# Performance work log

Hardware: AMD Instinct MI355X
Metric: run time of the kernel (lower is better)

## Reference

```python
import jax, jax.numpy as jnp
import numpy as np

B, NQ, NK = 2, 2048, 2048
QD, CD, H, DH = 1024, 768, 16, 64
INNER = H * DH


def setup_inputs() -> dict:
    key = jax.random.key(0)
    ks = jax.random.split(key, 8)
    x = jax.random.normal(ks[0], (B, NQ, QD), jnp.float32)
    context = jax.random.normal(ks[1], (B, NK, CD), jnp.float32)
    mask = jax.random.randint(ks[2], (B, 1, NQ, NK), 0, 2) > 0
    s = lambda d: 1.0 / np.sqrt(d)
    Wq = jax.random.normal(ks[3], (INNER, QD), jnp.float32) * s(QD)
    Wk = jax.random.normal(ks[4], (INNER, CD), jnp.float32) * s(CD)
    Wv = jax.random.normal(ks[5], (INNER, CD), jnp.float32) * s(CD)
    Wo = jax.random.normal(ks[6], (QD, INNER), jnp.float32) * s(INNER)
    bo = jax.random.normal(ks[7], (QD,), jnp.float32) * 0.01
    return {"x": x, "context": context, "mask": mask,
            "Wq": Wq, "Wk": Wk, "Wv": Wv, "Wo": Wo, "bo": bo}


def reference(x, context, mask, Wq, Wk, Wv, Wo, bo):
    scale = DH ** -0.5
    # QKV projections (Linear, no bias): [b, n, inner] -> [b, n, h, d]
    q = (x @ Wq.T).reshape(B, NQ, H, DH)
    k = (context @ Wk.T).reshape(B, NK, H, DH)
    v = (context @ Wv.T).reshape(B, NK, H, DH)
    # additive bias built from boolean mask (masked_fill with -finfo.max/2)
    max_neg = -jnp.finfo(q.dtype).max / 2
    bias = jnp.where(mask, jnp.zeros((), q.dtype), max_neg)  # [b,1,nq,nk]
    scores = jnp.einsum('bqhd,bkhd->bhqk', q, k) * scale + bias
    attn = jax.nn.softmax(scores, axis=-1)
    out = jnp.einsum('bhqk,bkhd->bqhd', attn, v).reshape(B, NQ, INNER)
    return out @ Wo.T + bo
```

## Files before the change

### kernel.cpp

```cpp
#include <hip/hip_runtime.h>
#include <float.h>
#include <stdint.h>

#define C_B     2
#define C_NQ    2048
#define C_NK    2048
#define C_QD    1024
#define C_CD    768
#define C_H     16
#define C_DH    64
#define C_INNER 1024

typedef __bf16 bf16;
typedef __attribute__((ext_vector_type(8))) __bf16 bf16x8;
typedef __attribute__((ext_vector_type(4))) __bf16 bf16x4;
typedef __attribute__((ext_vector_type(4))) float f32x4;
typedef __attribute__((ext_vector_type(16))) float f32x16;

#if __has_builtin(__builtin_amdgcn_exp2f)
#define EXP2(x) __builtin_amdgcn_exp2f(x)
#else
#define EXP2(x) __expf((x) * 0.69314718056f)
#endif

__device__ __forceinline__ void async_copy16(const bf16* g, bf16* l) {
  __builtin_amdgcn_global_load_lds(
      (const __attribute__((address_space(1))) void*)g,
      (__attribute__((address_space(3))) void*)l,
      16, 0, 0);
}

__global__ __launch_bounds__(256) void prep(const float* __restrict__ s0, const float* __restrict__ s1,
                                            const float* __restrict__ s2, const float* __restrict__ s3,
                                            const float* __restrict__ s4, const float* __restrict__ s5,
                                            bf16* __restrict__ d0, bf16* __restrict__ d1,
                                            bf16* __restrict__ d2, bf16* __restrict__ d3,
                                            bf16* __restrict__ d4, bf16* __restrict__ d5,
                                            const int* __restrict__ mask,
                                            unsigned long long* __restrict__ mb) {
  const int stride = gridDim.x * blockDim.x;
  for (int idx = blockIdx.x * blockDim.x + threadIdx.x; idx < 2752512; idx += stride) {
    const float* src; bf16* dst; int loc;
    if      (idx < 1048576) { src = s0; dst = d0; loc = idx; }
    else if (idx < 1835008) { src = s1; dst = d1; loc = idx - 1048576; }
    else if (idx < 2097152) { src = s2; dst = d2; loc = idx - 1835008; }
    else if (idx < 2293760) { src = s3; dst = d3; loc = idx - 2097152; }
    else if (idx < 2490368) { src = s4; dst = d4; loc = idx - 2293760; }
    else                    { src = s5; dst = d5; loc = idx - 2490368; }
    float4 f = *(const float4*)&src[loc * 4];
    bf16x4 o = { (bf16)f.x, (bf16)f.y, (bf16)f.z, (bf16)f.w };
    *(bf16x4*)&dst[loc * 4] = o;
  }
  const int lane = threadIdx.x & 63;
  const int wid  = (blockIdx.x * blockDim.x + threadIdx.x) >> 6;
  const int nw   = (gridDim.x * blockDim.x) >> 6;
  for (int w = wid; w < 131072; w += nw) {
    int v = mask[(size_t)w * 64 + lane];
    unsigned long long bb = __ballot(v != 0);
    if (lane == 0) mb[w] = bb;
  }
}

__device__ __forceinline__ void gemm_core(const bf16* __restrict__ A,
                                          const bf16* __restrict__ W,
                                          int m0, int n0, int K,
                                          bf16* As0, bf16* As1, bf16* Bs0, bf16* Bs1,
                                          f32x4 (&acc)[4][4],
                                          int w, int lane) {
  const int l15 = lane & 15, lg = lane >> 4;
  const int wm = w >> 1, wn = w & 1;
  bf16* AsA[2] = {As0, As1};
  bf16* BsA[2] = {Bs0, Bs1};

  auto stage = [&](int nb, int k0) {
#pragma unroll
    for (int i = 0; i < 2; ++i) {
      const int chunk = w * 128 + i * 64 + lane;
      const int row = chunk >> 2;
      const int srcb = ((chunk & 3) ^ (row & 3)) * 8;
      async_copy16(A + (size_t)(m0 + row) * K + k0 + srcb, &AsA[nb][chunk * 8]);
      async_copy16(W + (size_t)(n0 + row) * K + k0 + srcb, &BsA[nb][chunk * 8]);
    }
  };

  stage(0, 0);
  int cur = 0;
  for (int k0 = 0; k0 < K; k0 += 32) {
    __syncthreads();
    if (k0 + 32 < K) stage(cur ^ 1, k0 + 32);

    bf16x8 af[4], bfv[4];
#pragma unroll
    for (int mi = 0; mi < 4; ++mi) {
      const int row = wm * 64 + mi * 16 + l15;
      af[mi] = *(const bf16x8*)&AsA[cur][row * 32 + ((lg ^ (row & 3)) * 8)];
    }
#pragma unroll
    for (int ni = 0; ni < 4; ++ni) {
      const int row = wn * 64 + ni * 16 + l15;
      bfv[ni] = *(const bf16x8*)&BsA[cur][row * 32 + ((lg ^ (row & 3)) * 8)];
    }
#pragma unroll
    for (int mi = 0; mi < 4; ++mi)
#pragma unroll
      for (int ni = 0; ni < 4; ++ni)
        acc[mi][ni] = __builtin_amdgcn_mfma_f32_16x16x32_bf16(af[mi], bfv[ni],
                                                              acc[mi][ni], 0, 0, 0);
    cur ^= 1;
  }
}

__global__ __launch_bounds__(256) void gemm_qkv(const bf16* __restrict__ xb,
                                                const bf16* __restrict__ wqb,
                                                bf16* __restrict__ Qb,
                                                const bf16* __restrict__ cb,
                                                const bf16* __restrict__ wkv,
                                                bf16* __restrict__ Kb,
                                                bf16* __restrict__ Vb,
                                                float qscale) {
  __shared__ __align__(16) bf16 As[2][128 * 32];
  __shared__ __align__(16) bf16 Bs[2][128 * 32];

  const int bid = blockIdx.x;
  const int t = threadIdx.x, w = t >> 6, lane = t & 63;
  const int l15 = lane & 15, lg = lane >> 4;
  const int wm = w >> 1, wn = w & 1;

  const bf16 *A, *W;
  int m0, n0, K;
  float oscale;
  if (bid < 256) {
    A = xb; W = wqb; n0 = (bid & 7) * 128; m0 = (bid >> 3) * 128;
    K = C_QD; oscale = qscale;
  } else {
    const int b2 = bid - 256;
    A = cb; W = wkv; n0 = (b2 & 15) * 128; m0 = (b2 >> 4) * 128;
    K = C_CD; oscale = 1.0f;
  }

  f32x4 acc[4][4] = {};
  gemm_core(A, W, m0, n0, K, As[0], As[1], Bs[0], Bs[1], acc, w, lane);

#pragma unroll
  for (int mi = 0; mi < 4; ++mi)
#pragma unroll
    for (int ni = 0; ni < 4; ++ni)
#pragma unroll
      for (int r = 0; r < 4; ++r) {
        const int row = m0 + wm * 64 + mi * 16 + lg * 4 + r;
        const int col = n0 + wn * 64 + ni * 16 + l15;
        const float v = acc[mi][ni][r] * oscale;
        bf16* dst; int cc;
        if (bid < 256)            { dst = Qb; cc = col; }
        else if (col < C_INNER)   { dst = Kb; cc = col; }
        else                      { dst = Vb; cc = col - C_INNER; }
        dst[(size_t)row * C_INNER + cc] = (bf16)v;
      }
}

__global__ __launch_bounds__(256) void gemm_out(const bf16* __restrict__ A,
                                                const bf16* __restrict__ W,
                                                const float* __restrict__ bias,
                                                float* __restrict__ Cout,
                                                int M, int N, int K) {
  __shared__ __align__(16) bf16 As[2][64 * 32];
  __shared__ __align__(16) bf16 Bs[2][128 * 32];
  const int t = threadIdx.x, w = t >> 6, lane = t & 63;
  const int l15 = lane & 15, lg = lane >> 4;
  const int wm = w >> 1, wn = w & 1;
  const int m0 = blockIdx.y * 64, n0 = blockIdx.x * 128;

  f32x4 acc[2][4] = {};

  auto stage = [&](int nb, int k0) {
    {
      const int ca = w * 64 + lane;
      const int arow = ca >> 2;
      const int asrc = ((ca & 3) ^ (arow & 3)) * 8;
      async_copy16(A + (size_t)(m0 + arow) * K + k0 + asrc, &As[nb][ca * 8]);
    }
#pragma unroll
    for (int i = 0; i < 2; ++i) {
      const int cbk = w * 128 + i * 64 + lane;
      const int brow = cbk >> 2;
      const int bsrc = ((cbk & 3) ^ (brow & 3)) * 8;
      async_copy16(W + (size_t)(n0 + brow) * K + k0 + bsrc, &Bs[nb][cbk * 8]);
    }
  };

  stage(0, 0);
  int cur = 0;
  for (int k0 = 0; k0 < K; k0 += 32) {
    __syncthreads();
    if (k0 + 32 < K) stage(cur ^ 1, k0 + 32);

    bf16x8 af[2], bfv[4];
#pragma unroll
    for (int mi = 0; mi < 2; ++mi) {
      const int row = wm * 32 + mi * 16 + l15;
      af[mi] = *(const bf16x8*)&As[cur][row * 32 + ((lg ^ (row & 3)) * 8)];
    }
#pragma unroll
    for (int ni = 0; ni < 4; ++ni) {
      const int row = wn * 64 + ni * 16 + l15;
      bfv[ni] = *(const bf16x8*)&Bs[cur][row * 32 + ((lg ^ (row & 3)) * 8)];
    }
#pragma unroll
    for (int mi = 0; mi < 2; ++mi)
#pragma unroll
      for (int ni = 0; ni < 4; ++ni)
        acc[mi][ni] = __builtin_amdgcn_mfma_f32_16x16x32_bf16(af[mi], bfv[ni],
                                                              acc[mi][ni], 0, 0, 0);
    cur ^= 1;
  }

#pragma unroll
  for (int mi = 0; mi < 2; ++mi)
#pragma unroll
    for (int ni = 0; ni < 4; ++ni)
#pragma unroll
      for (int r = 0; r < 4; ++r) {
        const int row = m0 + wm * 32 + mi * 16 + lg * 4 + r;
        const int col = n0 + wn * 64 + ni * 16 + l15;
        Cout[(size_t)row * N + col] = acc[mi][ni][r] + bias[col];
      }
}

__global__ __launch_bounds__(256) void vtrans(const bf16* __restrict__ V,
                                              bf16* __restrict__ Vt) {
  __shared__ __align__(16) bf16 T[64][80];
  const int kt = blockIdx.x, h = blockIdx.y, b = blockIdx.z;
  const int t = threadIdx.x;
  {
    const int kl = t >> 2, db = (t & 3) * 16;
    const bf16* src = &V[((size_t)(b * C_NK + kt * 64 + kl)) * C_INNER + h * 64 + db];
    *(bf16x8*)&T[kl][db]     = *(const bf16x8*)&src[0];
    *(bf16x8*)&T[kl][db + 8] = *(const bf16x8*)&src[8];
  }
  __syncthreads();
  {
    const int d = t >> 2, kb = (t & 3) * 16;
    const int P0[8] = {0, 1, 2, 3, 8, 9, 10, 11};
    const int P1[8] = {4, 5, 6, 7, 12, 13, 14, 15};
    bf16x8 o0, o1;
#pragma unroll
    for (int j = 0; j < 8; ++j) { o0[j] = T[kb + P0[j]][d]; o1[j] = T[kb + P1[j]][d]; }
    bf16* dst = &Vt[((size_t)((b * C_H + h) * C_DH + d)) * C_NK + kt * 64 + kb];
    *(bf16x8*)&dst[0] = o0;
    *(bf16x8*)&dst[8] = o1;
  }
}

__global__ __launch_bounds__(256, 4) void attn_fwd(const bf16* __restrict__ Q,
                                                   const bf16* __restrict__ K,
                                                   const bf16* __restrict__ Vt,
                                                   const unsigned long long* __restrict__ MB,
                                                   bf16* __restrict__ O0,
                                                   bf16* __restrict__ O1,
                                                   float* __restrict__ L) {
  __shared__ __align__(16) bf16 Ks[2][64 * 64];
  __shared__ __align__(16) bf16 Vs[2][64 * 64];

  const int bid = blockIdx.x;
  const int swz = ((bid & 7) << 7) | (bid >> 3);
  const int qt = swz & 15, h = (swz >> 4) & 15, zz = swz >> 8;
  const int half = zz >> 1, b = zz & 1;
  const int t = threadIdx.x, wq = t >> 6, lane = t & 63;
  const int l31 = lane & 31, hi = lane >> 5;
  const int q = qt * 128 + wq * 32 + l31;

  bf16x8 qf[4];
  {
    const bf16* qp = Q + ((size_t)(b * C_NQ + q)) * C_INNER + h * C_DH;
#pragma unroll
    for (int db = 0; db < 4; ++db)
      qf[db] = *(const bf16x8*)&qp[db * 16 + hi * 8];
  }

  float l_run = 0.f;
  f32x16 acc_o[2] = {};

  auto stage = [&](int nb, int ktA) {
#pragma unroll
    for (int i = 0; i < 2; ++i) {
      const int chunk = wq * 128 + i * 64 + lane;
      const int row = chunk >> 3, pcb = chunk & 7;
      const int srcb = (pcb ^ (row & 7)) * 8;
      const bf16* kg = K + ((size_t)(b * C_NK + ktA * 64 + row)) * C_INNER + h * C_DH + srcb;
      async_copy16(kg, &Ks[nb][chunk * 8]);
      const bf16* vg = Vt + ((size_t)((b * C_H + h) * C_DH + row)) * C_NK + ktA * 64 + srcb;
      async_copy16(vg, &Vs[nb][chunk * 8]);
    }
  };

  const int kt0 = half * 16;
  stage(0, kt0);
  int cur = 0;

  for (int i = 0; i < 16; ++i) {
    const int ktA = kt0 + i;
    const unsigned long long wd =
        MB[((size_t)(b * C_NQ + q)) * (C_NK / 64) + ktA] >> (hi * 4);
    const unsigned mlo = (unsigned)wd, mhi = (unsigned)(wd >> 32);

    __syncthreads();
    if (i + 1 < 16) stage(cur ^ 1, ktA + 1);

    f32x16 s[2] = {};
    __builtin_amdgcn_s_setprio(1);
#pragma unroll
    for (int kb = 0; kb < 2; ++kb)
#pragma unroll
      for (int db = 0; db < 4; ++db) {
        const int row = kb * 32 + l31;
        const int cb = (db * 2 + hi) ^ (row & 7);
        bf16x8 kf = *(const bf16x8*)&Ks[cur][row * 64 + cb * 8];
        s[kb] = __builtin_amdgcn_mfma_f32_32x32x16_bf16(kf, qf[db], s[kb], 0, 0, 0);
      }
    __builtin_amdgcn_s_setprio(0);

    bf16x8 pfr[4];
    float psb[4];
#pragma unroll
    for (int kb = 0; kb < 2; ++kb) {
      const unsigned mw = kb ? mhi : mlo;
#pragma unroll
      for (int kss = 0; kss < 2; ++kss) {
        bf16x8 pf;
        float pv[8];
#pragma unroll
        for (int j = 0; j < 8; ++j) {
          const int reg = kss * 8 + j;
          const int pos = (reg & 3) + 8 * (reg >> 2);
          float p = EXP2(s[kb][reg]);
          p = ((mw >> pos) & 1u) ? p : 0.f;
          pv[j] = p;
          pf[j] = (bf16)p;
        }
        psb[kb * 2 + kss] = ((pv[0] + pv[1]) + (pv[2] + pv[3])) +
                            ((pv[4] + pv[5]) + (pv[6] + pv[7]));
        pfr[kb * 2 + kss] = pf;
      }
    }
    l_run += (psb[0] + psb[1]) + (psb[2] + psb[3]);

    __builtin_amdgcn_s_setprio(1);
#pragma unroll
    for (int ks = 0; ks < 4; ++ks) {
#pragma unroll
      for (int d2 = 0; d2 < 2; ++d2) {
        const int row = d2 * 32 + l31;
        const int cb = (ks * 2 + hi) ^ (row & 7);
        bf16x8 vf = *(const bf16x8*)&Vs[cur][row * 64 + cb * 8];
        acc_o[d2] = __builtin_amdgcn_mfma_f32_32x32x16_bf16(vf, pfr[ks], acc_o[d2], 0, 0, 0);
      }
    }
    __builtin_amdgcn_s_setprio(0);
    cur ^= 1;
  }

  {
    const float l_tot = l_run + __shfl_xor(l_run, 32);
    const size_t row = (size_t)(b * C_H + h) * C_NQ + q;
    bf16* op = (half ? O1 : O0) + row * 64;
#pragma unroll
    for (int d2 = 0; d2 < 2; ++d2)
#pragma unroll
      for (int bb = 0; bb < 4; ++bb) {
        bf16x4 o;
#pragma unroll
        for (int rr = 0; rr < 4; ++rr)
          o[rr] = (bf16)(acc_o[d2][bb * 4 + rr]);
        *(bf16x4*)&op[d2 * 32 + bb * 8 + hi * 4] = o;
      }
    if (hi == 0) L[(size_t)half * 65536 + row] = l_tot;
  }
}

__global__ __launch_bounds__(256) void merge_halves(const bf16* __restrict__ O0,
                                                    const bf16* __restrict__ O1,
                                                    const float* __restrict__ L,
                                                    bf16* __restrict__ AO) {
  const int t = threadIdx.x;
  const int r = blockIdx.x * 32 + (t >> 3);
  const int dc = (t & 7) * 8;
  const float inv = 1.0f / (L[r] + L[65536 + r]);
  bf16x8 a = *(const bf16x8*)&O0[(size_t)r * 64 + dc];
  bf16x8 c = *(const bf16x8*)&O1[(size_t)r * 64 + dc];
  bf16x8 o;
#pragma unroll
  for (int j = 0; j < 8; ++j)
    o[j] = (bf16)(((float)a[j] + (float)c[j]) * inv);
  const int q = r & 2047, bh = r >> 11, hh = bh & 15, bb = bh >> 4;
  *(bf16x8*)&AO[((size_t)(bb * C_NQ + q)) * C_INNER + hh * 64 + dc] = o;
}

extern "C" void kernel_launch(void* const* d_in, const int* in_sizes, int n_in,
                              void* d_out, int out_size, void* d_ws, size_t ws_size,
                              hipStream_t stream) {
  const float* x   = (const float*)d_in[0];
  const float* ctx = (const float*)d_in[1];
  const int*   msk = (const int*)d_in[2];
  const float* Wq  = (const float*)d_in[3];
  const float* Wk  = (const float*)d_in[4];
  const float* Wv  = (const float*)d_in[5];
  const float* Wo  = (const float*)d_in[6];
  const float* bo  = (const float*)d_in[7];
  float* out = (float*)d_out;

  bf16* ws  = (bf16*)d_ws;
  bf16* xb  = ws;
  bf16* cb  = xb  + 4194304;
  bf16* wqb = cb  + 3145728;
  bf16* wkb = wqb + 1048576;
  bf16* wvb = wkb + 786432;
  bf16* wob = wvb + 786432;
  bf16* Qb  = wob + 1048576;
  bf16* Kb  = Qb  + 4194304;
  bf16* Vb  = Kb  + 4194304;
  bf16* AOb = Vb  + 4194304;
  unsigned long long* mb = (unsigned long long*)(AOb + 4194304);
  float* lbuf = (float*)(mb + 131072);
  bf16* Vtb = xb;
  bf16* O0  = cb;
  bf16* O1  = Vb;

  dim3 blk(256);
  prep<<<2048, blk, 0, stream>>>(x, ctx, Wq, Wk, Wv, Wo,
                                 xb, cb, wqb, wkb, wvb, wob, msk, mb);

  const float qscale = 0.125f * 1.44269504f;
  gemm_qkv<<<768, blk, 0, stream>>>(xb, wqb, Qb, cb, wkb, Kb, Vb, qscale);

  vtrans<<<dim3(C_NK / 64, C_H, C_B), blk, 0, stream>>>(Vb, Vtb);

  attn_fwd<<<1024, blk, 0, stream>>>(Qb, Kb, Vtb, mb, O0, O1, lbuf);

  merge_halves<<<2048, blk, 0, stream>>>(O0, O1, lbuf, AOb);

  const int MQ = C_B * C_NQ;
  gemm_out<<<dim3(C_QD / 128, MQ / 64), blk, 0, stream>>>(
      AOb, wob, bo, out, MQ, C_QD, C_INNER);
}
```

Baseline: 144.9 us.

## Software-pipeline attention QK with PV across tiles and shrink QKV GEMM tile

The attention loop now computes QK scores for tile i while doing exp, masking and the PV MFMAs for tile i-1. V is triple-buffered in shared memory so its tile stays live one iteration longer, and occupancy is lowered from 4 to 3 blocks per CU to make room for the extra registers. The QKV projection GEMM switches to 64x128 tiles with twice as many blocks, sharing one core with the output GEMM, to improve CU fill. The cost is more register and LDS pressure in attention and more redundant weight loads in the QKV GEMM.

```diff
diff --git a/kernel.cpp b/kernel.cpp
--- a/kernel.cpp
+++ b/kernel.cpp
@@ -61,25 +61,30 @@
   }
 }
 
-__device__ __forceinline__ void gemm_core(const bf16* __restrict__ A,
-                                          const bf16* __restrict__ W,
-                                          int m0, int n0, int K,
-                                          bf16* As0, bf16* As1, bf16* Bs0, bf16* Bs1,
-                                          f32x4 (&acc)[4][4],
-                                          int w, int lane) {
+__device__ __forceinline__ void gemm64_core(const bf16* __restrict__ A,
+                                            const bf16* __restrict__ W,
+                                            int m0, int n0, int K,
+                                            bf16* As0, bf16* As1, bf16* Bs0, bf16* Bs1,
+                                            f32x4 (&acc)[2][4],
+                                            int w, int lane) {
   const int l15 = lane & 15, lg = lane >> 4;
   const int wm = w >> 1, wn = w & 1;
   bf16* AsA[2] = {As0, As1};
   bf16* BsA[2] = {Bs0, Bs1};
 
   auto stage = [&](int nb, int k0) {
+    {
+      const int ca = w * 64 + lane;
+      const int arow = ca >> 2;
+      const int asrc = ((ca & 3) ^ (arow & 3)) * 8;
+      async_copy16(A + (size_t)(m0 + arow) * K + k0 + asrc, &AsA[nb][ca * 8]);
+    }
 #pragma unroll
     for (int i = 0; i < 2; ++i) {
-      const int chunk = w * 128 + i * 64 + lane;
-      const int row = chunk >> 2;
-      const int srcb = ((chunk & 3) ^ (row & 3)) * 8;
-      async_copy16(A + (size_t)(m0 + row) * K + k0 + srcb, &AsA[nb][chunk * 8]);
-      async_copy16(W + (size_t)(n0 + row) * K + k0 + srcb, &BsA[nb][chunk * 8]);
+      const int cbk = w * 128 + i * 64 + lane;
+      const int brow = cbk >> 2;
+      const int bsrc = ((cbk & 3) ^ (brow & 3)) * 8;
+      async_copy16(W + (size_t)(n0 + brow) * K + k0 + bsrc, &BsA[nb][cbk * 8]);
     }
   };
 
@@ -89,10 +94,10 @@
     __syncthreads();
     if (k0 + 32 < K) stage(cur ^ 1, k0 + 32);
 
-    bf16x8 af[4], bfv[4];
-#pragma unroll
-    for (int mi = 0; mi < 4; ++mi) {
-      const int row = wm * 64 + mi * 16 + l15;
+    bf16x8 af[2], bfv[4];
+#pragma unroll
+    for (int mi = 0; mi < 2; ++mi) {
+      const int row = wm * 32 + mi * 16 + l15;
       af[mi] = *(const bf16x8*)&AsA[cur][row * 32 + ((lg ^ (row & 3)) * 8)];
     }
 #pragma unroll
@@ -101,7 +106,7 @@
       bfv[ni] = *(const bf16x8*)&BsA[cur][row * 32 + ((lg ^ (row & 3)) * 8)];
     }
 #pragma unroll
-    for (int mi = 0; mi < 4; ++mi)
+    for (int mi = 0; mi < 2; ++mi)
 #pragma unroll
       for (int ni = 0; ni < 4; ++ni)
         acc[mi][ni] = __builtin_amdgcn_mfma_f32_16x16x32_bf16(af[mi], bfv[ni],
@@ -118,7 +123,7 @@
                                                 bf16* __restrict__ Kb,
                                                 bf16* __restrict__ Vb,
                                                 float qscale) {
-  __shared__ __align__(16) bf16 As[2][128 * 32];
+  __shared__ __align__(16) bf16 As[2][64 * 32];
   __shared__ __align__(16) bf16 Bs[2][128 * 32];
 
   const int bid = blockIdx.x;
@@ -129,29 +134,29 @@
   const bf16 *A, *W;
   int m0, n0, K;
   float oscale;
-  if (bid < 256) {
-    A = xb; W = wqb; n0 = (bid & 7) * 128; m0 = (bid >> 3) * 128;
+  if (bid < 512) {
+    A = xb; W = wqb; n0 = (bid & 7) * 128; m0 = (bid >> 3) * 64;
     K = C_QD; oscale = qscale;
   } else {
-    const int b2 = bid - 256;
-    A = cb; W = wkv; n0 = (b2 & 15) * 128; m0 = (b2 >> 4) * 128;
+    const int b2 = bid - 512;
+    A = cb; W = wkv; n0 = (b2 & 15) * 128; m0 = (b2 >> 4) * 64;
     K = C_CD; oscale = 1.0f;
   }
 
-  f32x4 acc[4][4] = {};
-  gemm_core(A, W, m0, n0, K, As[0], As[1], Bs[0], Bs[1], acc, w, lane);
-
-#pragma unroll
-  for (int mi = 0; mi < 4; ++mi)
+  f32x4 acc[2][4] = {};
+  gemm64_core(A, W, m0, n0, K, As[0], As[1], Bs[0], Bs[1], acc, w, lane);
+
+#pragma unroll
+  for (int mi = 0; mi < 2; ++mi)
 #pragma unroll
     for (int ni = 0; ni < 4; ++ni)
 #pragma unroll
       for (int r = 0; r < 4; ++r) {
-        const int row = m0 + wm * 64 + mi * 16 + lg * 4 + r;
+        const int row = m0 + wm * 32 + mi * 16 + lg * 4 + r;
         const int col = n0 + wn * 64 + ni * 16 + l15;
         const float v = acc[mi][ni][r] * oscale;
         bf16* dst; int cc;
-        if (bid < 256)            { dst = Qb; cc = col; }
+        if (bid < 512)            { dst = Qb; cc = col; }
         else if (col < C_INNER)   { dst = Kb; cc = col; }
         else                      { dst = Vb; cc = col - C_INNER; }
         dst[(size_t)row * C_INNER + cc] = (bf16)v;
@@ -171,48 +176,7 @@
   const int m0 = blockIdx.y * 64, n0 = blockIdx.x * 128;
 
   f32x4 acc[2][4] = {};
-
-  auto stage = [&](int nb, int k0) {
-    {
-      const int ca = w * 64 + lane;
-      const int arow = ca >> 2;
-      const int asrc = ((ca & 3) ^ (arow & 3)) * 8;
-      async_copy16(A + (size_t)(m0 + arow) * K + k0 + asrc, &As[nb][ca * 8]);
-    }
-#pragma unroll
-    for (int i = 0; i < 2; ++i) {
-      const int cbk = w * 128 + i * 64 + lane;
-      const int brow = cbk >> 2;
-      const int bsrc = ((cbk & 3) ^ (brow & 3)) * 8;
-      async_copy16(W + (size_t)(n0 + brow) * K + k0 + bsrc, &Bs[nb][cbk * 8]);
-    }
-  };
-
-  stage(0, 0);
-  int cur = 0;
-  for (int k0 = 0; k0 < K; k0 += 32) {
-    __syncthreads();
-    if (k0 + 32 < K) stage(cur ^ 1, k0 + 32);
-
-    bf16x8 af[2], bfv[4];
-#pragma unroll
-    for (int mi = 0; mi < 2; ++mi) {
-      const int row = wm * 32 + mi * 16 + l15;
-      af[mi] = *(const bf16x8*)&As[cur][row * 32 + ((lg ^ (row & 3)) * 8)];
-    }
-#pragma unroll
-    for (int ni = 0; ni < 4; ++ni) {
-      const int row = wn * 64 + ni * 16 + l15;
-      bfv[ni] = *(const bf16x8*)&Bs[cur][row * 32 + ((lg ^ (row & 3)) * 8)];
-    }
-#pragma unroll
-    for (int mi = 0; mi < 2; ++mi)
-#pragma unroll
-      for (int ni = 0; ni < 4; ++ni)
-        acc[mi][ni] = __builtin_amdgcn_mfma_f32_16x16x32_bf16(af[mi], bfv[ni],
-                                                              acc[mi][ni], 0, 0, 0);
-    cur ^= 1;
-  }
+  gemm64_core(A, W, m0, n0, K, As[0], As[1], Bs[0], Bs[1], acc, w, lane);
 
 #pragma unroll
   for (int mi = 0; mi < 2; ++mi)
@@ -251,7 +215,7 @@
   }
 }
 
-__global__ __launch_bounds__(256, 4) void attn_fwd(const bf16* __restrict__ Q,
+__global__ __launch_bounds__(256, 3) void attn_fwd(const bf16* __restrict__ Q,
                                                    const bf16* __restrict__ K,
                                                    const bf16* __restrict__ Vt,
                                                    const unsigned long long* __restrict__ MB,
@@ -259,7 +223,7 @@
                                                    bf16* __restrict__ O1,
                                                    float* __restrict__ L) {
   __shared__ __align__(16) bf16 Ks[2][64 * 64];
-  __shared__ __align__(16) bf16 Vs[2][64 * 64];
+  __shared__ __align__(16) bf16 Vs[3][64 * 64];
 
   const int bid = blockIdx.x;
   const int swz = ((bid & 7) << 7) | (bid >> 3);
@@ -279,51 +243,44 @@
 
   float l_run = 0.f;
   f32x16 acc_o[2] = {};
-
-  auto stage = [&](int nb, int ktA) {
+  f32x16 s2[2][2];
+
+  const size_t mrow = (size_t)(b * C_NQ + q) * (C_NK / 64);
+
+  auto stage = [&](int ktA, int kb, int vb) {
 #pragma unroll
     for (int i = 0; i < 2; ++i) {
       const int chunk = wq * 128 + i * 64 + lane;
       const int row = chunk >> 3, pcb = chunk & 7;
       const int srcb = (pcb ^ (row & 7)) * 8;
       const bf16* kg = K + ((size_t)(b * C_NK + ktA * 64 + row)) * C_INNER + h * C_DH + srcb;
-      async_copy16(kg, &Ks[nb][chunk * 8]);
+      async_copy16(kg, &Ks[kb][chunk * 8]);
       const bf16* vg = Vt + ((size_t)((b * C_H + h) * C_DH + row)) * C_NK + ktA * 64 + srcb;
-      async_copy16(vg, &Vs[nb][chunk * 8]);
+      async_copy16(vg, &Vs[vb][chunk * 8]);
     }
   };
 
-  const int kt0 = half * 16;
-  stage(0, kt0);
-  int cur = 0;
-
-  for (int i = 0; i < 16; ++i) {
-    const int ktA = kt0 + i;
-    const unsigned long long wd =
-        MB[((size_t)(b * C_NQ + q)) * (C_NK / 64) + ktA] >> (hi * 4);
-    const unsigned mlo = (unsigned)wd, mhi = (unsigned)(wd >> 32);
-
-    __syncthreads();
-    if (i + 1 < 16) stage(cur ^ 1, ktA + 1);
-
-    f32x16 s[2] = {};
+  auto qk = [&](f32x16 (&s)[2], int kb) {
+    s[0] = (f32x16){};
+    s[1] = (f32x16){};
     __builtin_amdgcn_s_setprio(1);
 #pragma unroll
-    for (int kb = 0; kb < 2; ++kb)
+    for (int kbb = 0; kbb < 2; ++kbb)
 #pragma unroll
       for (int db = 0; db < 4; ++db) {
-        const int row = kb * 32 + l31;
+        const int row = kbb * 32 + l31;
         const int cb = (db * 2 + hi) ^ (row & 7);
-        bf16x8 kf = *(const bf16x8*)&Ks[cur][row * 64 + cb * 8];
-        s[kb] = __builtin_amdgcn_mfma_f32_32x32x16_bf16(kf, qf[db], s[kb], 0, 0, 0);
+        bf16x8 kf = *(const bf16x8*)&Ks[kb][row * 64 + cb * 8];
+        s[kbb] = __builtin_amdgcn_mfma_f32_32x32x16_bf16(kf, qf[db], s[kbb], 0, 0, 0);
       }
     __builtin_amdgcn_s_setprio(0);
-
-    bf16x8 pfr[4];
-    float psb[4];
-#pragma unroll
-    for (int kb = 0; kb < 2; ++kb) {
-      const unsigned mw = kb ? mhi : mlo;
+  };
+
+  auto packpv = [&](f32x16 (&s)[2], unsigned long long wd, int vb) {
+    const unsigned mlo = (unsigned)wd, mhi = (unsigned)(wd >> 32);
+#pragma unroll
+    for (int kbb = 0; kbb < 2; ++kbb) {
+      const unsigned mw = kbb ? mhi : mlo;
 #pragma unroll
       for (int kss = 0; kss < 2; ++kss) {
         bf16x8 pf;
@@ -332,32 +289,44 @@
         for (int j = 0; j < 8; ++j) {
           const int reg = kss * 8 + j;
           const int pos = (reg & 3) + 8 * (reg >> 2);
-          float p = EXP2(s[kb][reg]);
+          float p = EXP2(s[kbb][reg]);
           p = ((mw >> pos) & 1u) ? p : 0.f;
           pv[j] = p;
           pf[j] = (bf16)p;
         }
-        psb[kb * 2 + kss] = ((pv[0] + pv[1]) + (pv[2] + pv[3])) +
-                            ((pv[4] + pv[5]) + (pv[6] + pv[7]));
-        pfr[kb * 2 + kss] = pf;
+        l_run += ((pv[0] + pv[1]) + (pv[2] + pv[3])) +
+                 ((pv[4] + pv[5]) + (pv[6] + pv[7]));
+        const int ks = kbb * 2 + kss;
+        __builtin_amdgcn_s_setprio(1);
+#pragma unroll
+        for (int d2 = 0; d2 < 2; ++d2) {
+          const int row = d2 * 32 + l31;
+          const int cb = (ks * 2 + hi) ^ (row & 7);
+          bf16x8 vf = *(const bf16x8*)&Vs[vb][row * 64 + cb * 8];
+          acc_o[d2] = __builtin_amdgcn_mfma_f32_32x32x16_bf16(vf, pf, acc_o[d2], 0, 0, 0);
+        }
+        __builtin_amdgcn_s_setprio(0);
       }
     }
-    l_run += (psb[0] + psb[1]) + (psb[2] + psb[3]);
-
-    __builtin_amdgcn_s_setprio(1);
-#pragma unroll
-    for (int ks = 0; ks < 4; ++ks) {
-#pragma unroll
-      for (int d2 = 0; d2 < 2; ++d2) {
-        const int row = d2 * 32 + l31;
-        const int cb = (ks * 2 + hi) ^ (row & 7);
-        bf16x8 vf = *(const bf16x8*)&Vs[cur][row * 64 + cb * 8];
-        acc_o[d2] = __builtin_amdgcn_mfma_f32_32x32x16_bf16(vf, pfr[ks], acc_o[d2], 0, 0, 0);
-      }
-    }
-    __builtin_amdgcn_s_setprio(0);
-    cur ^= 1;
-  }
+  };
+
+  const int kt0 = half * 16;
+  stage(kt0, 0, 0);
+  unsigned long long wd_prev = MB[mrow + kt0] >> (hi * 4);
+  __syncthreads();
+  stage(kt0 + 1, 1, 1);
+  qk(s2[0], 0);
+
+#pragma unroll
+  for (int i = 1; i < 16; ++i) {
+    const unsigned long long wd_cur = MB[mrow + kt0 + i] >> (hi * 4);
+    __syncthreads();
+    if (i + 1 < 16) stage(kt0 + i + 1, (i + 1) & 1, (i + 1) % 3);
+    qk(s2[i & 1], i & 1);
+    packpv(s2[(i - 1) & 1], wd_prev, (i - 1) % 3);
+    wd_prev = wd_cur;
+  }
+  packpv(s2[1], wd_prev, 0);
 
   {
     const float l_tot = l_run + __shfl_xor(l_run, 32);
@@ -430,7 +399,7 @@
                                  xb, cb, wqb, wkb, wvb, wob, msk, mb);
 
   const float qscale = 0.125f * 1.44269504f;
-  gemm_qkv<<<768, blk, 0, stream>>>(xb, wqb, Qb, cb, wkb, Kb, Vb, qscale);
+  gemm_qkv<<<1536, blk, 0, stream>>>(xb, wqb, Qb, cb, wkb, Kb, Vb, qscale);
 
   vtrans<<<dim3(C_NK / 64, C_H, C_B), blk, 0, stream>>>(Vb, Vtb);
 
```

After: 162.2 us. 1.12x slower.

## Fuse split-K attention merge into output projection GEMM A-tile loading

Applied to the files above, without the earlier changes.

Drops the separate merge_halves kernel. The output GEMM now loads both partial attention outputs and the softmax denominators, combines and normalizes them in registers, and writes the bf16 result straight into shared memory as the A tile. This saves one launch and a full write and read of the merged attention buffer. In exchange the A tile is now a synchronous global load plus arithmetic instead of an async copy, which may stall the GEMM pipeline and repeats the merge work for every column block. The attention loop also prefetches the next mask word one iteration ahead.

```diff
diff --git a/kernel.cpp b/kernel.cpp
--- a/kernel.cpp
+++ b/kernel.cpp
@@ -158,11 +158,13 @@
       }
 }
 
-__global__ __launch_bounds__(256) void gemm_out(const bf16* __restrict__ A,
-                                                const bf16* __restrict__ W,
-                                                const float* __restrict__ bias,
-                                                float* __restrict__ Cout,
-                                                int M, int N, int K) {
+__global__ __launch_bounds__(256) void gemm_out_fused(const bf16* __restrict__ O0,
+                                                      const bf16* __restrict__ O1,
+                                                      const float* __restrict__ L,
+                                                      const bf16* __restrict__ W,
+                                                      const float* __restrict__ bias,
+                                                      float* __restrict__ Cout,
+                                                      int M, int N, int K) {
   __shared__ __align__(16) bf16 As[2][64 * 32];
   __shared__ __align__(16) bf16 Bs[2][128 * 32];
   const int t = threadIdx.x, w = t >> 6, lane = t & 63;
@@ -172,27 +174,41 @@
 
   f32x4 acc[2][4] = {};
 
-  auto stage = [&](int nb, int k0) {
-    {
-      const int ca = w * 64 + lane;
-      const int arow = ca >> 2;
-      const int asrc = ((ca & 3) ^ (arow & 3)) * 8;
-      async_copy16(A + (size_t)(m0 + arow) * K + k0 + asrc, &As[nb][ca * 8]);
-    }
+  const int ca = w * 64 + lane;
+  const int arow = ca >> 2;
+  const int asrcb = ((ca & 3) ^ (arow & 3)) * 8;
+  const int grow = m0 + arow;
+  const int gb = grow >> 11, gq = grow & 2047;
+
+  auto stageA = [&](bf16* dstA, int k0) {
+    const int col = k0 + asrcb;
+    const int hh = col >> 6, d = col & 63;
+    const size_t r = (size_t)(gb * C_H + hh) * C_NQ + gq;
+    bf16x8 o0 = *(const bf16x8*)&O0[r * 64 + d];
+    bf16x8 o1 = *(const bf16x8*)&O1[r * 64 + d];
+    const float inv = 1.0f / (L[r] + L[65536 + r]);
+    bf16x8 av;
+#pragma unroll
+    for (int j = 0; j < 8; ++j)
+      av[j] = (bf16)(((float)o0[j] + (float)o1[j]) * inv);
+    *(bf16x8*)&dstA[ca * 8] = av;
+  };
+  auto stageB = [&](bf16* dstB, int k0) {
 #pragma unroll
     for (int i = 0; i < 2; ++i) {
       const int cbk = w * 128 + i * 64 + lane;
       const int brow = cbk >> 2;
       const int bsrc = ((cbk & 3) ^ (brow & 3)) * 8;
-      async_copy16(W + (size_t)(n0 + brow) * K + k0 + bsrc, &Bs[nb][cbk * 8]);
+      async_copy16(W + (size_t)(n0 + brow) * K + k0 + bsrc, &dstB[cbk * 8]);
     }
   };
 
-  stage(0, 0);
+  stageA(As[0], 0);
+  stageB(Bs[0], 0);
   int cur = 0;
   for (int k0 = 0; k0 < K; k0 += 32) {
     __syncthreads();
-    if (k0 + 32 < K) stage(cur ^ 1, k0 + 32);
+    if (k0 + 32 < K) { stageA(As[cur ^ 1], k0 + 32); stageB(Bs[cur ^ 1], k0 + 32); }
 
     bf16x8 af[2], bfv[4];
 #pragma unroll
@@ -279,6 +295,7 @@
 
   float l_run = 0.f;
   f32x16 acc_o[2] = {};
+  const size_t mrow = (size_t)(b * C_NQ + q) * (C_NK / 64);
 
   auto stage = [&](int nb, int ktA) {
 #pragma unroll
@@ -295,16 +312,15 @@
 
   const int kt0 = half * 16;
   stage(0, kt0);
+  unsigned long long wd = MB[mrow + kt0] >> (hi * 4);
   int cur = 0;
 
   for (int i = 0; i < 16; ++i) {
-    const int ktA = kt0 + i;
-    const unsigned long long wd =
-        MB[((size_t)(b * C_NQ + q)) * (C_NK / 64) + ktA] >> (hi * 4);
+    __syncthreads();
+    if (i + 1 < 16) stage(cur ^ 1, kt0 + i + 1);
+    unsigned long long wd_next = 0;
+    if (i + 1 < 16) wd_next = MB[mrow + kt0 + i + 1] >> (hi * 4);
     const unsigned mlo = (unsigned)wd, mhi = (unsigned)(wd >> 32);
-
-    __syncthreads();
-    if (i + 1 < 16) stage(cur ^ 1, ktA + 1);
 
     f32x16 s[2] = {};
     __builtin_amdgcn_s_setprio(1);
@@ -356,6 +372,7 @@
       }
     }
     __builtin_amdgcn_s_setprio(0);
+    wd = wd_next;
     cur ^= 1;
   }
 
@@ -375,24 +392,6 @@
       }
     if (hi == 0) L[(size_t)half * 65536 + row] = l_tot;
   }
-}
-
-__global__ __launch_bounds__(256) void merge_halves(const bf16* __restrict__ O0,
-                                                    const bf16* __restrict__ O1,
-                                                    const float* __restrict__ L,
-                                                    bf16* __restrict__ AO) {
-  const int t = threadIdx.x;
-  const int r = blockIdx.x * 32 + (t >> 3);
-  const int dc = (t & 7) * 8;
-  const float inv = 1.0f / (L[r] + L[65536 + r]);
-  bf16x8 a = *(const bf16x8*)&O0[(size_t)r * 64 + dc];
-  bf16x8 c = *(const bf16x8*)&O1[(size_t)r * 64 + dc];
-  bf16x8 o;
-#pragma unroll
-  for (int j = 0; j < 8; ++j)
-    o[j] = (bf16)(((float)a[j] + (float)c[j]) * inv);
-  const int q = r & 2047, bh = r >> 11, hh = bh & 15, bb = bh >> 4;
-  *(bf16x8*)&AO[((size_t)(bb * C_NQ + q)) * C_INNER + hh * 64 + dc] = o;
 }
 
 extern "C" void kernel_launch(void* const* d_in, const int* in_sizes, int n_in,
@@ -436,9 +435,7 @@
 
   attn_fwd<<<1024, blk, 0, stream>>>(Qb, Kb, Vtb, mb, O0, O1, lbuf);
 
-  merge_halves<<<2048, blk, 0, stream>>>(O0, O1, lbuf, AOb);
-
   const int MQ = C_B * C_NQ;
-  gemm_out<<<dim3(C_QD / 128, MQ / 64), blk, 0, stream>>>(
-      AOb, wob, bo, out, MQ, C_QD, C_INNER);
-}
+  gemm_out_fused<<<dim3(C_QD / 128, MQ / 64), blk, 0, stream>>>(
+      O0, O1, lbuf, wob, bo, out, MQ, C_QD, C_INNER);
+}
```

Measured after the change: 156.5 us. 8.0% more time.
